# Kernel optimization log

Hardware: AMD Instinct MI355X
Metric: run time of the kernel (lower is better)

## Reference

```python
import jax, jax.numpy as jnp
from jax import lax
import numpy as np

HEAD_SIZE = 64
D_MIX = 32
D_DECAY = 64
D_GATE = 64


def setup_inputs() -> dict:
    key = jax.random.key(0)
    B, T, C = 4, 2048, 1024
    H = C // HEAD_SIZE
    ks = jax.random.split(key, 24)
    n = lambda i, shape, s=1.0: (jax.random.normal(ks[i], shape, dtype=jnp.float32) * s)
    return {
        "x": n(0, (B, T, C)),
        "maa_x": n(1, (C,), 0.1), "maa_w": n(2, (C,), 0.1), "maa_k": n(3, (C,), 0.1),
        "maa_v": n(4, (C,), 0.1), "maa_r": n(5, (C,), 0.1), "maa_g": n(6, (C,), 0.1),
        "maa_w1": n(7, (C, 5 * D_MIX), 0.01), "maa_w2": n(8, (5, D_MIX, C), 0.01),
        "Wr": n(9, (C, C), C ** -0.5), "Wk": n(10, (C, C), C ** -0.5),
        "Wv": n(11, (C, C), C ** -0.5), "Wo": n(12, (C, C), C ** -0.5),
        "gate_w1": n(13, (C, D_GATE), 0.01), "gate_w2": n(14, (D_GATE, C), 0.01),
        "time_decay": n(15, (C,), 1.0) - 4.0,
        "decay_w1": n(16, (C, D_DECAY), 0.01), "decay_w2": n(17, (D_DECAY, C), 0.01),
        "u": n(18, (H, HEAD_SIZE), 0.1),
        "ln_g": jnp.ones((C,), jnp.float32), "ln_b": jnp.zeros((C,), jnp.float32),
    }


def _wkv6(r, k, v, w, u):
    # r,k,v: [B,T,C]; w: decay (already exp(-exp(.))) [B,T,C]; u: [H,N]
    B, T, C = r.shape
    N = HEAD_SIZE
    H = C // N
    to_h = lambda a: a.reshape(B, T, H, N).transpose(1, 0, 2, 3)  # [T,B,H,N]
    rT, kT, vT, wT = map(to_h, (r, k, v, w))

    def step(S, inp):  # S: [B,H,N,N] (key_dim i x value_dim j)
        rt, kt, vt, wt = inp
        kv = kt[..., :, None] * vt[..., None, :]            # [B,H,N,N]
        y = jnp.einsum('bhi,bhij->bhj', rt, S + u[None, :, :, None] * kv)
        S = wt[..., None] * S + kv
        return S, y

    S0 = jnp.zeros((B, H, N, N), r.dtype)
    _, y = lax.scan(step, S0, (rT, kT, vT, wT))
    return y.transpose(1, 0, 2, 3).reshape(B, T, C)


def reference(x, maa_x, maa_w, maa_k, maa_v, maa_r, maa_g, maa_w1, maa_w2,
              Wr, Wk, Wv, Wo, gate_w1, gate_w2, time_decay, decay_w1, decay_w2,
              u, ln_g, ln_b):
    B, T, C = x.shape
    H, N = C // HEAD_SIZE, HEAD_SIZE
    # time shift: prepend zero row, drop last (ZeroPad2d((0,0,1,-1)))
    xx = jnp.concatenate([jnp.zeros_like(x[:, :1]), x[:, :-1]], axis=1) - x
    xxx = x + xx * maa_x
    lora = jnp.tanh(xxx @ maa_w1).reshape(B, T, 5, D_MIX)
    m = jnp.einsum('btfd,fdc->fbtc', lora, maa_w2)  # [5,B,T,C]
    mw, mk, mv, mr, mg = m[0], m[1], m[2], m[3], m[4]
    xw = x + xx * (maa_w + mw)
    xk = x + xx * (maa_k + mk)
    xv = x + xx * (maa_v + mv)
    xr = x + xx * (maa_r + mr)
    xg = x + xx * (maa_g + mg)
    r = xr @ Wr
    k = xk @ Wk
    v = xv @ Wv
    g = jnp.tanh(xg @ gate_w1) @ gate_w2
    w = time_decay + jnp.tanh(xw @ decay_w1) @ decay_w2
    wdec = jnp.exp(-jnp.exp(w))  # decay applied inside the CUDA kernel
    y = _wkv6(r, k, v, wdec, u)
    # GroupNorm over heads, eps = 1e-5 * HEAD_SIZE_DIVISOR**2 = 6.4e-4
    yh = y.reshape(B, T, H, N)
    mu = yh.mean(-1, keepdims=True)
    var = yh.var(-1, keepdims=True)
    yn = ((yh - mu) / jnp.sqrt(var + 6.4e-4)).reshape(B, T, C) * ln_g + ln_b
    return (yn * g) @ Wo
```

## Files before the change

### kernel.cpp

```cpp
#include <hip/hip_runtime.h>
#include <hip/hip_bf16.h>
#include <stdint.h>

typedef __hip_bfloat16 bf16;
typedef __attribute__((ext_vector_type(8))) short bf16x8;
typedef __attribute__((ext_vector_type(4))) float f32x4;

#define CC 1024
#define TT 2048
#define BB 4
#define BT 8192
#define HH 16
#define NN 64

#define MFMA(a, b, c) __builtin_amdgcn_mfma_f32_16x16x32_bf16(a, b, c, 0, 0, 0)

#define GLD(g, l) __builtin_amdgcn_global_load_lds( \
    (const __attribute__((address_space(1))) void*)(g), \
    (__attribute__((address_space(3))) void*)(l), 16, 0, 0)

__device__ __forceinline__ short f2bs(float f) {
    bf16 h = __float2bfloat16(f);
    return *reinterpret_cast<short*>(&h);
}
__device__ __forceinline__ float bs2f(short s) {
    bf16 h = *reinterpret_cast<bf16*>(&s);
    return __bfloat162float(h);
}

__device__ __forceinline__ size_t blk_idx(int m, int k, int ktiles) {
    return ((size_t)(m >> 8) * ktiles + (k >> 6)) * 16384
         + ((k >> 3) & 7) * 2048 + (m & 255) * 8 + (k & 7);
}

template <typename EPI>
__device__ __forceinline__ void gemm128(short* As, short* Bs,
                                        const bf16* __restrict__ A, int lda,
                                        const bf16* __restrict__ Bt, int ldb,
                                        int kiters, int m0, int n0, EPI epi)
{
    const int tid = threadIdx.x;
    const int l   = tid & 63, wv = tid >> 6;
    const int wm  = wv >> 1, wn = wv & 1;
    const int q   = l >> 4, lr = l & 15;
    const int row = tid & 127, kg1 = tid >> 7;

    f32x4 acc[4][4] = {};

    const bf16* ga = A  + (size_t)(m0 + row) * lda + kg1 * 8;
    const bf16* gb = Bt + (size_t)(n0 + row) * ldb + kg1 * 8;
    short* la1 = As + tid * 8;
    short* la2 = As + (tid + 256) * 8;
    short* lb1 = Bs + tid * 8;
    short* lb2 = Bs + (tid + 256) * 8;

    for (int kb = 0; kb < kiters; ++kb) {
        __syncthreads();
        const bf16* gak = ga + kb * 32;
        const bf16* gbk = gb + kb * 32;
        GLD(gak,      la1);
        GLD(gak + 16, la2);
        GLD(gbk,      lb1);
        GLD(gbk + 16, lb2);
        __syncthreads();
        bf16x8 af[4], bfb[4];
#pragma unroll
        for (int mt = 0; mt < 4; ++mt)
            af[mt] = *(const bf16x8*)(As + (q * 128 + wm * 64 + mt * 16 + lr) * 8);
#pragma unroll
        for (int nt = 0; nt < 4; ++nt)
            bfb[nt] = *(const bf16x8*)(Bs + (q * 128 + wn * 64 + nt * 16 + lr) * 8);
#pragma unroll
        for (int mt = 0; mt < 4; ++mt)
#pragma unroll
            for (int nt = 0; nt < 4; ++nt)
                acc[mt][nt] = MFMA(af[mt], bfb[nt], acc[mt][nt]);
    }
#pragma unroll
    for (int mt = 0; mt < 4; ++mt)
#pragma unroll
        for (int nt = 0; nt < 4; ++nt)
#pragma unroll
            for (int rr = 0; rr < 4; ++rr)
                epi(m0 + wm * 64 + mt * 16 + q * 4 + rr,
                    n0 + wn * 64 + nt * 16 + lr, acc[mt][nt][rr]);
}

template <typename EPI>
__device__ __forceinline__ void gemm128k64(short* As, short* Bs,
                                           const bf16* __restrict__ A, int lda,
                                           const bf16* __restrict__ Bt, int ldb,
                                           int kiters, int m0, int n0, EPI epi)
{
    const int tid = threadIdx.x;
    const int l   = tid & 63, wv = tid >> 6;
    const int wm  = wv >> 1, wn = wv & 1;
    const int q   = l >> 4, lr = l & 15;
    const int row = tid & 127, kg1 = tid >> 7;

    f32x4 acc[4][4] = {};

    const bf16* ga = A  + (size_t)(m0 + row) * lda + kg1 * 8;
    const bf16* gb = Bt + (size_t)(n0 + row) * ldb + kg1 * 8;

    auto stage = [&](int kb, int u) {
        const bf16* gak = ga + kb * 64;
        const bf16* gbk = gb + kb * 64;
        short* la = As + u * 8192 + tid * 8;
        short* lb = Bs + u * 8192 + tid * 8;
        GLD(gak,      la);
        GLD(gak + 16, la + 2048);
        GLD(gak + 32, la + 4096);
        GLD(gak + 48, la + 6144);
        GLD(gbk,      lb);
        GLD(gbk + 16, lb + 2048);
        GLD(gbk + 32, lb + 4096);
        GLD(gbk + 48, lb + 6144);
    };

    __syncthreads();
    stage(0, 0);
    __syncthreads();
    for (int kb = 0; kb < kiters; ++kb) {
        const int cur = kb & 1;
        if (kb + 1 < kiters) stage(kb + 1, cur ^ 1);
        const short* Ac = As + cur * 8192;
        const short* Bc = Bs + cur * 8192;
        bf16x8 af[2][4], bfb[2][4];
#pragma unroll
        for (int hh = 0; hh < 2; ++hh) {
#pragma unroll
            for (int mt = 0; mt < 4; ++mt)
                af[hh][mt] = *(const bf16x8*)(Ac +
                    ((q + hh * 4) * 128 + wm * 64 + mt * 16 + lr) * 8);
#pragma unroll
            for (int nt = 0; nt < 4; ++nt)
                bfb[hh][nt] = *(const bf16x8*)(Bc +
                    ((q + hh * 4) * 128 + wn * 64 + nt * 16 + lr) * 8);
        }
        __builtin_amdgcn_s_setprio(1);
#pragma unroll
        for (int mt = 0; mt < 4; ++mt)
#pragma unroll
            for (int nt = 0; nt < 4; ++nt) {
                acc[mt][nt] = MFMA(af[0][mt], bfb[0][nt], acc[mt][nt]);
                acc[mt][nt] = MFMA(af[1][mt], bfb[1][nt], acc[mt][nt]);
            }
        __builtin_amdgcn_s_setprio(0);
        __syncthreads();
    }
#pragma unroll
    for (int mt = 0; mt < 4; ++mt)
#pragma unroll
        for (int nt = 0; nt < 4; ++nt)
#pragma unroll
            for (int rr = 0; rr < 4; ++rr)
                epi(m0 + wm * 64 + mt * 16 + q * 4 + rr,
                    n0 + wn * 64 + nt * 16 + lr, acc[mt][nt][rr]);
}

template <typename EPI>
__device__ __forceinline__ void gemm256(short* As, short* Bs,
                                        const bf16* __restrict__ A,
                                        const bf16* __restrict__ Bt,
                                        int kiters, int m0, int n0, EPI epi)
{
    const int tid = threadIdx.x;
    const int l   = tid & 63, wv = tid >> 6;
    const int wm  = wv >> 2, wn = wv & 3;
    const int q   = l >> 4, lr = l & 15;

    f32x4 acc[8][4] = {};

    const bf16* ga = A  + (size_t)(m0 >> 8) * 16 * 16384 + tid * 8;
    const bf16* gb = Bt + (size_t)(n0 >> 8) * 16 * 16384 + tid * 8;

    auto stage = [&](int kb, int u) {
        const bf16* gak = ga + (size_t)kb * 16384;
        const bf16* gbk = gb + (size_t)kb * 16384;
        short* la = As + u * 16384 + tid * 8;
        short* lb = Bs + u * 16384 + tid * 8;
        GLD(gak,         la);
        GLD(gak + 4096,  la + 4096);
        GLD(gak + 8192,  la + 8192);
        GLD(gak + 12288, la + 12288);
        GLD(gbk,         lb);
        GLD(gbk + 4096,  lb + 4096);
        GLD(gbk + 8192,  lb + 8192);
        GLD(gbk + 12288, lb + 12288);
    };

    __syncthreads();
    stage(0, 0);
    __syncthreads();
    for (int kb = 0; kb < kiters; ++kb) {
        const int cur = kb & 1;
        if (kb + 1 < kiters) stage(kb + 1, cur ^ 1);
        const short* Ac = As + cur * 16384;
        const short* Bc = Bs + cur * 16384;
#pragma unroll
        for (int hh = 0; hh < 2; ++hh) {
            bf16x8 af[8], bfb[4];
#pragma unroll
            for (int mt = 0; mt < 8; ++mt)
                af[mt] = *(const bf16x8*)(Ac +
                    ((q + hh * 4) * 256 + wm * 128 + mt * 16 + lr) * 8);
#pragma unroll
            for (int nt = 0; nt < 4; ++nt)
                bfb[nt] = *(const bf16x8*)(Bc +
                    ((q + hh * 4) * 256 + wn * 64 + nt * 16 + lr) * 8);
            __builtin_amdgcn_s_setprio(1);
#pragma unroll
            for (int mt = 0; mt < 8; ++mt)
#pragma unroll
                for (int nt = 0; nt < 4; ++nt)
                    acc[mt][nt] = MFMA(af[mt], bfb[nt], acc[mt][nt]);
            __builtin_amdgcn_s_setprio(0);
        }
        __syncthreads();
    }
#pragma unroll
    for (int mt = 0; mt < 8; ++mt)
#pragma unroll
        for (int nt = 0; nt < 4; ++nt)
#pragma unroll
            for (int rr = 0; rr < 4; ++rr)
                epi(m0 + wm * 128 + mt * 16 + q * 4 + rr,
                    n0 + wn * 64 + nt * 16 + lr, acc[mt][nt][rr]);
}

template <typename EPI>
__device__ __forceinline__ void gemmHid(short* As, short* Bs,
                                        const bf16* __restrict__ A,
                                        const bf16* __restrict__ Bt, int ldb,
                                        int kiters, int m0, EPI epi)
{
    const int tid = threadIdx.x;
    const int l   = tid & 63, wv = tid >> 6;
    const int q   = l >> 4, lr = l & 15;
    const int row64 = tid & 63, kg8 = tid >> 6;

    f32x4 acc[2][4] = {};

    const bf16* ga = A + (size_t)(m0 >> 8) * 16 * 16384 + tid * 8;
    const bf16* gb = Bt + (size_t)row64 * ldb + kg8 * 8;

    auto stage = [&](int kb, int u) {
        const bf16* gak = ga + (size_t)kb * 16384;
        short* la = As + u * 16384 + tid * 8;
        GLD(gak,         la);
        GLD(gak + 4096,  la + 4096);
        GLD(gak + 8192,  la + 8192);
        GLD(gak + 12288, la + 12288);
        GLD(gb + kb * 64, Bs + u * 4096 + tid * 8);
    };

    __syncthreads();
    stage(0, 0);
    __syncthreads();
    for (int kb = 0; kb < kiters; ++kb) {
        const int cur = kb & 1;
        if (kb + 1 < kiters) stage(kb + 1, cur ^ 1);
        const short* Ac = As + cur * 16384;
        const short* Bc = Bs + cur * 4096;
        bf16x8 af[2][2], bfb[2][4];
#pragma unroll
        for (int hh = 0; hh < 2; ++hh) {
#pragma unroll
            for (int mt = 0; mt < 2; ++mt)
                af[hh][mt] = *(const bf16x8*)(Ac +
                    ((q + hh * 4) * 256 + wv * 32 + mt * 16 + lr) * 8);
#pragma unroll
            for (int nt = 0; nt < 4; ++nt)
                bfb[hh][nt] = *(const bf16x8*)(Bc +
                    ((q + hh * 4) * 64 + nt * 16 + lr) * 8);
        }
#pragma unroll
        for (int mt = 0; mt < 2; ++mt)
#pragma unroll
            for (int nt = 0; nt < 4; ++nt) {
                acc[mt][nt] = MFMA(af[0][mt], bfb[0][nt], acc[mt][nt]);
                acc[mt][nt] = MFMA(af[1][mt], bfb[1][nt], acc[mt][nt]);
            }
        __syncthreads();
    }
#pragma unroll
    for (int mt = 0; mt < 2; ++mt)
#pragma unroll
        for (int nt = 0; nt < 4; ++nt)
#pragma unroll
            for (int rr = 0; rr < 4; ++rr)
                epi(m0 + wv * 32 + mt * 16 + q * 4 + rr,
                    nt * 16 + lr, acc[mt][nt][rr]);
}

__global__ __launch_bounds__(256) void k_prep_all(
    const float* __restrict__ Wr, const float* __restrict__ Wk,
    const float* __restrict__ Wv, const float* __restrict__ Wo,
    const float* __restrict__ maa_w1, const float* __restrict__ gate_w1,
    const float* __restrict__ decay_w1, const float* __restrict__ gate_w2,
    const float* __restrict__ decay_w2, const float* __restrict__ maa_w2,
    const float* __restrict__ mw, const float* __restrict__ mk,
    const float* __restrict__ mv, const float* __restrict__ mr,
    const float* __restrict__ mg, const float* __restrict__ x,
    const float* __restrict__ maa_x,
    bf16* __restrict__ WT3, bf16* __restrict__ WoT, bf16* __restrict__ w1T,
    bf16* __restrict__ w1T2, bf16* __restrict__ w2T2, bf16* __restrict__ w2T5,
    float* __restrict__ maas, bf16* __restrict__ xxx,
    bf16* __restrict__ xb, bf16* __restrict__ xxb)
{
    __shared__ float tile[32][33];
    int idx = blockIdx.x;
    if (idx >= 4900) {
        size_t i = ((size_t)(idx - 4900) * 256 + threadIdx.x) * 4;
        int cc = i & (CC - 1);
        int t  = (i >> 10) & (TT - 1);
        float4 xm = *(const float4*)(x + i);
        float4 xp = t ? *(const float4*)(x + i - CC)
                      : make_float4(0.f, 0.f, 0.f, 0.f);
        float4 ax = *(const float4*)(maa_x + cc);
        float xxv[4] = {xp.x - xm.x, xp.y - xm.y, xp.z - xm.z, xp.w - xm.w};
        float xmv[4] = {xm.x, xm.y, xm.z, xm.w};
        float axv[4] = {ax.x, ax.y, ax.z, ax.w};
#pragma unroll
        for (int e = 0; e < 4; ++e) {
            xb[i + e]  = __float2bfloat16(xmv[e]);
            xxb[i + e] = __float2bfloat16(xxv[e]);
            xxx[i + e] = __float2bfloat16(xmv[e] + xxv[e] * axv[e]);
        }
        return;
    }
    const float* src; bf16* dst; int rows, cols_in, tx_;
    bool blocked = false;
    if (idx < 4096) {
        int s = idx >> 10; idx &= 1023;
        src = (s == 0) ? Wr : (s == 1) ? Wk : (s == 2) ? Wv : Wo;
        dst = (s == 3) ? WoT : WT3 + (size_t)s * CC * CC;
        blocked = (s != 3);
        rows = CC; cols_in = CC; tx_ = 32;
    } else if (idx < 4352) { idx -= 4096; src = maa_w1;  dst = w1T;  rows = CC; cols_in = 160; tx_ = 8; }
    else if (idx < 4480)   { idx -= 4352; src = gate_w1; dst = w1T2; rows = CC; cols_in = 64;  tx_ = 4; }
    else if (idx < 4608)   { idx -= 4480; src = decay_w1; dst = w1T2 + 128 * CC; rows = CC; cols_in = 64; tx_ = 4; }
    else if (idx < 4672)   { idx -= 4608; src = gate_w2;  dst = w2T2;           rows = 64; cols_in = CC; tx_ = 32; }
    else if (idx < 4736)   { idx -= 4672; src = decay_w2; dst = w2T2 + CC * 64; rows = 64; cols_in = CC; tx_ = 32; }
    else if (idx < 4896)   { idx -= 4736; int f = idx >> 5; idx &= 31;
                             src = maa_w2 + (size_t)f * 32 * CC;
                             dst = w2T5 + (size_t)f * CC * 32; rows = 32; cols_in = CC; tx_ = 32; }
    else {
        int i = (idx - 4896) * 256 + threadIdx.x;
        if (i < CC) {
            maas[i]          = mw[i];
            maas[CC + i]     = mk[i];
            maas[2 * CC + i] = mv[i];
            maas[3 * CC + i] = mr[i];
            maas[4 * CC + i] = mg[i];
        }
        return;
    }
    int bx = idx % tx_, by = idx / tx_;
    int c0 = bx * 32, r0 = by * 32;
    int tx = threadIdx.x & 31, ty = threadIdx.x >> 5;
    for (int i = ty; i < 32; i += 8) {
        int cc2 = c0 + tx;
        tile[i][tx] = (cc2 < cols_in) ? src[(size_t)(r0 + i) * cols_in + cc2] : 0.f;
    }
    __syncthreads();
    if (blocked) {
        for (int i = ty; i < 32; i += 8) {
            int R = c0 + i, C = r0 + tx;
            dst[blk_idx(R, C, 16)] = __float2bfloat16(tile[tx][i]);
        }
    } else {
        for (int i = ty; i < 32; i += 8)
            dst[(size_t)(c0 + i) * rows + r0 + tx] = __float2bfloat16(tile[tx][i]);
    }
}

__global__ __launch_bounds__(256) void g_lora(const bf16* __restrict__ xxx,
                                              const bf16* __restrict__ w1T,
                                              bf16* __restrict__ L)
{
    __shared__ __align__(16) short lds[8192];
    int m0 = blockIdx.x * 128, n0 = blockIdx.y * 128;
    gemm128(lds, lds + 4096, xxx, CC, w1T, CC, CC / 32, m0, n0,
            [&](int m, int n, float v) {
                if (n < 160) L[(size_t)m * 160 + n] = __float2bfloat16(tanhf(v));
            });
}

__global__ __launch_bounds__(256) void g_xvar(const bf16* __restrict__ L,
                                              const bf16* __restrict__ w2T,
                                              const float* __restrict__ maas,
                                              const bf16* __restrict__ xb,
                                              const bf16* __restrict__ xxb,
                                              bf16* __restrict__ xvars)
{
    __shared__ __align__(16) short lds[8192];
    int m0 = blockIdx.x * 128, n0 = blockIdx.y * 128;
    for (int f = 0; f < 5; ++f) {
        const bf16* A  = L + f * 32;
        const bf16* Bt = w2T + (size_t)f * CC * 32;
        const float* maa = maas + f * CC;
        bf16* out = xvars + (size_t)f * BT * CC;
        gemm128(lds, lds + 4096, A, 160, Bt, 32, 1, m0, n0,
                [&](int m, int n, float v) {
                    float xm = __bfloat162float(xb[(size_t)m * CC + n]);
                    float xx = __bfloat162float(xxb[(size_t)m * CC + n]);
                    out[blk_idx(m, n, 16)] =
                        __float2bfloat16(xm + xx * (maa[n] + v));
                });
    }
}

__global__ __launch_bounds__(512) void g_rkv5(const bf16* __restrict__ xvars,
                                              const bf16* __restrict__ WT,
                                              const bf16* __restrict__ w1T2,
                                              bf16* __restrict__ rkv,
                                              bf16* __restrict__ hid)
{
    __shared__ __align__(16) short lds[65536];
    int bid = blockIdx.x;
    if (bid < 384) {
        int swz = (bid & 7) * 48 + (bid >> 3);
        int z  = swz >> 7;
        int r2 = swz & 127;
        int n0 = (r2 >> 5) * 256;
        int m0 = (r2 & 31) * 256;
        int f = (z == 0) ? 3 : z;
        const bf16* A  = xvars + (size_t)f * BT * CC;
        const bf16* Bt = WT + (size_t)z * CC * CC;
        bf16* out = rkv + (size_t)z * BT * CC;
        gemm256(lds, lds + 32768, A, Bt, CC / 64, m0, n0,
                [&](int m, int n, float v) {
                    out[(size_t)m * CC + n] = __float2bfloat16(v);
                });
    } else {
        int hb = bid - 384;
        int zz = hb >> 5, mi = hb & 31;
        const bf16* A  = xvars + (size_t)(zz == 0 ? 4 : 0) * BT * CC;
        const bf16* Bt = w1T2 + (size_t)zz * 128 * CC;
        bf16* out = hid + (size_t)zz * BT * 64;
        gemmHid(lds, lds + 32768, A, Bt, CC, CC / 64, mi * 256,
                [&](int m, int n, float v) {
                    out[(size_t)m * 64 + n] = __float2bfloat16(tanhf(v));
                });
    }
}

__global__ __launch_bounds__(256) void k_wkv_p1(const bf16* __restrict__ r,
                                                const bf16* __restrict__ kk,
                                                const bf16* __restrict__ vv,
                                                const bf16* __restrict__ hidW,
                                                const bf16* __restrict__ w2d,
                                                const float* __restrict__ td,
                                                const float* __restrict__ u,
                                                bf16* __restrict__ y,
                                                bf16* __restrict__ RTg,
                                                short* __restrict__ Mg,
                                                float* __restrict__ plg)
{
    constexpr int PW = 65, PB = 72;
    __shared__ __align__(16) char smem[16640 + 3 * 9216 + 768];
    float* LW = (float*)smem;
    short* VT = (short*)smem;
    short* RT = (short*)(smem + 16640);
    short* KT = (short*)(smem + 16640 + 9216);
    short* AT = KT;
    short* KH = (short*)(smem + 16640 + 2 * 9216);
    short* HT = KT;
    short* WD = KH;
    float* SU = (float*)(smem + 16640 + 3 * 9216);
    float* SD = SU + 64;

    const int tid = threadIdx.x;
    const int lane = tid & 63, wq = tid >> 6;
    const int row = tid >> 2, g = tid & 3, j0 = g * 16;
    const int l15 = lane & 15, q = lane >> 4;
    const int bh = blockIdx.x >> 5, c = blockIdx.x & 31;
    const int b = bh >> 4, h = bh & 15;
    const size_t base = (size_t)b * TT * CC + (size_t)h * NN;
    const int t0 = c * 64;
    const int bt0 = b * TT + t0;
    const size_t cb = (size_t)blockIdx.x * 4096;

    if (tid < 64) SU[tid] = u[h * NN + tid];

#pragma unroll
    for (int rnd = 0; rnd < 2; ++rnd) {
        int ee = rnd * 256 + tid;
        int rw = ee >> 3, c8 = (ee & 7) * 8;
        *(bf16x8*)(HT + rw * PB + c8) =
            *(const bf16x8*)(hidW + (size_t)(bt0 + rw) * 64 + c8);
        *(bf16x8*)(WD + rw * PB + c8) =
            *(const bf16x8*)(w2d + (size_t)(h * 64 + rw) * 64 + c8);
    }
    const size_t gb = base + (size_t)(t0 + row) * CC + j0;
    bf16x8 r0 = *(const bf16x8*)(r + gb),  r1 = *(const bf16x8*)(r + gb + 8);
    bf16x8 k0 = *(const bf16x8*)(kk + gb), k1 = *(const bf16x8*)(kk + gb + 8);
    bf16x8 v0 = *(const bf16x8*)(vv + gb), v1 = *(const bf16x8*)(vv + gb + 8);
    float tdv[4];
#pragma unroll
    for (int ct = 0; ct < 4; ++ct) tdv[ct] = td[h * 64 + ct * 16 + l15];
    __syncthreads();
    {
        bf16x8 aH0 = *(const bf16x8*)(HT + (wq * 16 + l15) * PB + q * 8);
        bf16x8 aH1 = *(const bf16x8*)(HT + (wq * 16 + l15) * PB + q * 8 + 32);
        f32x4 lwa[4] = {};
#pragma unroll
        for (int ct = 0; ct < 4; ++ct) {
            bf16x8 bW0 = *(const bf16x8*)(WD + (ct * 16 + l15) * PB + q * 8);
            bf16x8 bW1 = *(const bf16x8*)(WD + (ct * 16 + l15) * PB + q * 8 + 32);
            lwa[ct] = MFMA(aH0, bW0, lwa[ct]);
            lwa[ct] = MFMA(aH1, bW1, lwa[ct]);
        }
#pragma unroll
        for (int ct = 0; ct < 4; ++ct)
#pragma unroll
            for (int rr = 0; rr < 4; ++rr) {
                int t = wq * 16 + q * 4 + rr, j = ct * 16 + l15;
                LW[t * PW + j] = -expf(tdv[ct] + lwa[ct][rr]);
            }
    }
    __syncthreads();
    for (int jj = 0; jj < 16; ++jj) {
        int j = wq * 16 + jj;
        float xv = LW[lane * PW + j];
#pragma unroll
        for (int d = 1; d < 64; d <<= 1) {
            float t2 = __shfl_up(xv, d);
            if (lane >= d) xv += t2;
        }
        LW[lane * PW + j] = xv;
    }
    __syncthreads();
    float rF[16], kF[16];
#pragma unroll
    for (int c2 = 0; c2 < 8; ++c2) {
        rF[c2] = bs2f(r0[c2]); rF[8 + c2] = bs2f(r1[c2]);
        kF[c2] = bs2f(k0[c2]); kF[8 + c2] = bs2f(k1[c2]);
    }
    float cwp[16], cwm[16], cwL[16];
#pragma unroll
    for (int c2 = 0; c2 < 16; ++c2) {
        cwp[c2] = LW[row * PW + j0 + c2];
        cwm[c2] = row ? LW[(row - 1) * PW + j0 + c2] : 0.f;
        cwL[c2] = LW[63 * PW + j0 + c2];
    }
    bf16x8 w0, w1;
#pragma unroll
    for (int c2 = 0; c2 < 8; ++c2) {
        w0[c2] = f2bs(rF[c2] * expf(cwm[c2]));
        w1[c2] = f2bs(rF[8 + c2] * expf(cwm[8 + c2]));
    }
    *(bf16x8*)(RT + row * PB + j0)     = w0;
    *(bf16x8*)(RT + row * PB + j0 + 8) = w1;
    *(bf16x8*)((short*)RTg + cb + row * 64 + j0)     = w0;
    *(bf16x8*)((short*)RTg + cb + row * 64 + j0 + 8) = w1;
#pragma unroll
    for (int c2 = 0; c2 < 8; ++c2) {
        w0[c2] = f2bs(kF[c2] * expf(-cwp[c2]));
        w1[c2] = f2bs(kF[8 + c2] * expf(-cwp[8 + c2]));
    }
    *(bf16x8*)(KT + row * PB + j0)     = w0;
    *(bf16x8*)(KT + row * PB + j0 + 8) = w1;
#pragma unroll
    for (int c2 = 0; c2 < 16; ++c2)
        KH[(j0 + c2) * PB + row] = f2bs(kF[c2] * expf(cwL[c2] - cwp[c2]));
    if (tid < 64) plg[(size_t)blockIdx.x * 64 + tid] = expf(LW[63 * PW + tid]);
    float dpart = 0.f;
#pragma unroll
    for (int c2 = 0; c2 < 16; ++c2)
        dpart = fmaf(rF[c2] * kF[c2], SU[j0 + c2], dpart);
    dpart += __shfl_xor(dpart, 1);
    dpart += __shfl_xor(dpart, 2);
    if (g == 0) SD[row] = dpart;
    __syncthreads();
#pragma unroll
    for (int c2 = 0; c2 < 8; ++c2) {
        VT[(j0 + c2) * PB + row]     = v0[c2];
        VT[(j0 + 8 + c2) * PB + row] = v1[c2];
    }
    bf16x8 aF0 = *(const bf16x8*)(RT + (wq * 16 + l15) * PB + q * 8);
    bf16x8 aF1 = *(const bf16x8*)(RT + (wq * 16 + l15) * PB + q * 8 + 32);
    f32x4 Am[4] = {};
#pragma unroll
    for (int ct = 0; ct < 4; ++ct) {
        bf16x8 bF0 = *(const bf16x8*)(KT + (ct * 16 + l15) * PB + q * 8);
        bf16x8 bF1 = *(const bf16x8*)(KT + (ct * 16 + l15) * PB + q * 8 + 32);
        Am[ct] = MFMA(aF0, bF0, Am[ct]);
        Am[ct] = MFMA(aF1, bF1, Am[ct]);
    }
    __syncthreads();
#pragma unroll
    for (int ct = 0; ct < 4; ++ct)
#pragma unroll
        for (int rr = 0; rr < 4; ++rr) {
            int s = wq * 16 + q * 4 + rr, p = ct * 16 + l15;
            float vA = Am[ct][rr];
            vA = (p > s) ? 0.f : (p == s ? SD[s] : vA);
            AT[s * PB + p] = f2bs(vA);
        }
    __syncthreads();
    f32x4 Y[4] = {}, M[4] = {};
    bf16x8 aA0 = *(const bf16x8*)(AT + (wq * 16 + l15) * PB + q * 8);
    bf16x8 aA1 = *(const bf16x8*)(AT + (wq * 16 + l15) * PB + q * 8 + 32);
    bf16x8 aV0 = *(const bf16x8*)(VT + (wq * 16 + l15) * PB + q * 8);
    bf16x8 aV1 = *(const bf16x8*)(VT + (wq * 16 + l15) * PB + q * 8 + 32);
#pragma unroll
    for (int ct = 0; ct < 4; ++ct) {
        bf16x8 bV0 = *(const bf16x8*)(VT + (ct * 16 + l15) * PB + q * 8);
        bf16x8 bV1 = *(const bf16x8*)(VT + (ct * 16 + l15) * PB + q * 8 + 32);
        Y[ct] = MFMA(aA0, bV0, Y[ct]);
        Y[ct] = MFMA(aA1, bV1, Y[ct]);
        bf16x8 bK0 = *(const bf16x8*)(KH + (ct * 16 + l15) * PB + q * 8);
        bf16x8 bK1 = *(const bf16x8*)(KH + (ct * 16 + l15) * PB + q * 8 + 32);
        M[ct] = MFMA(aV0, bK0, M[ct]);
        M[ct] = MFMA(aV1, bK1, M[ct]);
    }
#pragma unroll
    for (int ct = 0; ct < 4; ++ct)
#pragma unroll
        for (int rr = 0; rr < 4; ++rr) {
            int s = wq * 16 + q * 4 + rr;
            y[base + (size_t)(t0 + s) * CC + ct * 16 + l15] =
                __float2bfloat16(Y[ct][rr]);
            Mg[cb + (size_t)s * 64 + ct * 16 + l15] = f2bs(M[ct][rr]);
        }
}

__global__ __launch_bounds__(256) void k_wkv_p2(const short* __restrict__ Mg,
                                                const float* __restrict__ plg,
                                                bf16* __restrict__ Sg)
{
    int bh = blockIdx.x >> 4, part = blockIdx.x & 15;
    int i = part * 4 + (threadIdx.x >> 6), j = threadIdx.x & 63;
    float S = 0.f;
    size_t eb = (size_t)bh * 32 * 4096 + (size_t)i * 64 + j;
    size_t pb = (size_t)bh * 32 * 64 + j;
    for (int c = 0; c < 32; ++c) {
        Sg[eb + (size_t)c * 4096] = __float2bfloat16(S);
        S = plg[pb + (size_t)c * 64] * S + bs2f(Mg[eb + (size_t)c * 4096]);
    }
}

__global__ __launch_bounds__(256) void k_wkv_p3(const bf16* __restrict__ RTg,
                                                const bf16* __restrict__ Sg,
                                                const bf16* __restrict__ y,
                                                const bf16* __restrict__ hidG,
                                                const bf16* __restrict__ w2g,
                                                const float* __restrict__ ln_g,
                                                const float* __restrict__ ln_b,
                                                bf16* __restrict__ A2)
{
    constexpr int PB = 72;
    __shared__ __align__(16) short BufA[64 * PB], BufB[64 * PB];
    const int tid = threadIdx.x;
    const int lane = tid & 63, wq = tid >> 6;
    const int l15 = lane & 15, q = lane >> 4;
    const int bh = blockIdx.x >> 5, c = blockIdx.x & 31;
    const int b = bh >> 4, h = bh & 15;
    const int t0 = c * 64;
    const int bt0 = b * TT + t0;
    const size_t cb = (size_t)blockIdx.x * 4096;

#pragma unroll
    for (int rnd = 0; rnd < 2; ++rnd) {
        int ee = rnd * 256 + tid;
        int rw = ee >> 3, c8 = (ee & 7) * 8;
        *(bf16x8*)(BufA + rw * PB + c8) =
            *(const bf16x8*)(hidG + (size_t)(bt0 + rw) * 64 + c8);
        *(bf16x8*)(BufB + rw * PB + c8) =
            *(const bf16x8*)(w2g + (size_t)(h * 64 + rw) * 64 + c8);
    }
    __syncthreads();
    f32x4 G[4] = {};
    {
        bf16x8 aH0 = *(const bf16x8*)(BufA + (wq * 16 + l15) * PB + q * 8);
        bf16x8 aH1 = *(const bf16x8*)(BufA + (wq * 16 + l15) * PB + q * 8 + 32);
#pragma unroll
        for (int ct = 0; ct < 4; ++ct) {
            bf16x8 bW0 = *(const bf16x8*)(BufB + (ct * 16 + l15) * PB + q * 8);
            bf16x8 bW1 = *(const bf16x8*)(BufB + (ct * 16 + l15) * PB + q * 8 + 32);
            G[ct] = MFMA(aH0, bW0, G[ct]);
            G[ct] = MFMA(aH1, bW1, G[ct]);
        }
    }
    __syncthreads();
#pragma unroll
    for (int rnd = 0; rnd < 2; ++rnd) {
        int ee = rnd * 256 + tid;
        int rw = ee >> 3, c8 = (ee & 7) * 8;
        *(bf16x8*)(BufA + rw * PB + c8) =
            *(const bf16x8*)((const short*)RTg + cb + rw * 64 + c8);
        *(bf16x8*)(BufB + rw * PB + c8) =
            *(const bf16x8*)((const short*)Sg + cb + rw * 64 + c8);
    }
    __syncthreads();

    f32x4 Yc[4];
#pragma unroll
    for (int ct = 0; ct < 4; ++ct)
#pragma unroll
        for (int rr = 0; rr < 4; ++rr) {
            int s = wq * 16 + q * 4 + rr;
            Yc[ct][rr] = __bfloat162float(
                y[((size_t)bt0 + s) * CC + h * NN + ct * 16 + l15]);
        }
    bf16x8 aF0 = *(const bf16x8*)(BufA + (wq * 16 + l15) * PB + q * 8);
    bf16x8 aF1 = *(const bf16x8*)(BufA + (wq * 16 + l15) * PB + q * 8 + 32);
#pragma unroll
    for (int ct = 0; ct < 4; ++ct) {
        bf16x8 bS0 = *(const bf16x8*)(BufB + (ct * 16 + l15) * PB + q * 8);
        bf16x8 bS1 = *(const bf16x8*)(BufB + (ct * 16 + l15) * PB + q * 8 + 32);
        Yc[ct] = MFMA(aF0, bS0, Yc[ct]);
        Yc[ct] = MFMA(aF1, bS1, Yc[ct]);
    }
#pragma unroll
    for (int rr = 0; rr < 4; ++rr) {
        float s1 = 0.f, s2 = 0.f;
#pragma unroll
        for (int ct = 0; ct < 4; ++ct) {
            float vA = Yc[ct][rr];
            s1 += vA; s2 += vA * vA;
        }
#pragma unroll
        for (int o = 1; o < 16; o <<= 1) {
            s1 += __shfl_xor(s1, o);
            s2 += __shfl_xor(s2, o);
        }
        float mu  = s1 * (1.f / 64.f);
        float var = s2 * (1.f / 64.f) - mu * mu;
        float rstd = rsqrtf(var + 6.4e-4f);
        int s = wq * 16 + q * 4 + rr;
        size_t mrow = ((size_t)bt0 + s) * CC;
#pragma unroll
        for (int ct = 0; ct < 4; ++ct) {
            int ch = h * NN + ct * 16 + l15;
            float yn = (Yc[ct][rr] - mu) * rstd;
            float out = (yn * ln_g[ch] + ln_b[ch]) * G[ct][rr];
            A2[mrow + ch] = __float2bfloat16(out);
        }
    }
}

__global__ __launch_bounds__(256) void g_out(const bf16* __restrict__ A2,
                                             const bf16* __restrict__ WoT,
                                             float* __restrict__ out)
{
    __shared__ __align__(16) short lds[32768];
    int m0 = blockIdx.x * 128, n0 = blockIdx.y * 128;
    gemm128k64(lds, lds + 16384, A2, CC, WoT, CC, CC / 64, m0, n0,
               [&](int m, int n, float v) { out[(size_t)m * CC + n] = v; });
}

extern "C" void kernel_launch(void* const* d_in, const int* in_sizes, int n_in,
                              void* d_out, int out_size, void* d_ws, size_t ws_size,
                              hipStream_t stream)
{
    const float* x        = (const float*)d_in[0];
    const float* maa_x    = (const float*)d_in[1];
    const float* maa_w    = (const float*)d_in[2];
    const float* maa_k    = (const float*)d_in[3];
    const float* maa_v    = (const float*)d_in[4];
    const float* maa_r    = (const float*)d_in[5];
    const float* maa_g    = (const float*)d_in[6];
    const float* maa_w1   = (const float*)d_in[7];
    const float* maa_w2   = (const float*)d_in[8];
    const float* Wr       = (const float*)d_in[9];
    const float* Wk       = (const float*)d_in[10];
    const float* Wv       = (const float*)d_in[11];
    const float* Wo       = (const float*)d_in[12];
    const float* gate_w1  = (const float*)d_in[13];
    const float* gate_w2  = (const float*)d_in[14];
    const float* time_dec = (const float*)d_in[15];
    const float* decay_w1 = (const float*)d_in[16];
    const float* decay_w2 = (const float*)d_in[17];
    const float* u        = (const float*)d_in[18];
    const float* ln_g     = (const float*)d_in[19];
    const float* ln_b     = (const float*)d_in[20];

    size_t off = 0;
    auto alloc = [&](size_t bytes) {
        off = (off + 255) & ~(size_t)255;
        void* p = (char*)d_ws + off;
        off += bytes;
        return p;
    };
    bf16*  WT3   = (bf16*) alloc(3ull * CC * CC * 2);
    bf16*  WoT   = (bf16*) alloc((size_t)CC * CC * 2);
    bf16*  w1T   = (bf16*) alloc(256ull * CC * 2);
    bf16*  w1T2  = (bf16*) alloc(2ull * 128 * CC * 2);
    bf16*  w2T2  = (bf16*) alloc(2ull * CC * 64 * 2);
    bf16*  w2T5  = (bf16*) alloc(5ull * CC * 32 * 2);
    float* maas  = (float*)alloc(5ull * CC * 4);
    char* bufA = (char*)alloc((size_t)BT * CC * 2);
    bf16* xxxbf = (bf16*)bufA;
    bf16* A2    = (bf16*)bufA;
    char* bufB = (char*)alloc((size_t)BT * 160 * 2);
    bf16* Lbf  = (bf16*)bufB;
    bf16* hid  = (bf16*)bufB;
    char* bufC = (char*)alloc(5ull * BT * CC * 2);
    bf16*  xvars = (bf16*)bufC;
    bf16*  ybuf  = (bf16*)bufC;
    bf16*  RTg   = (bf16*)(bufC + (size_t)BT * CC * 2);
    bf16*  rkv  = (bf16*)alloc(3ull * BT * CC * 2);
    bf16*  Sg   = rkv;
    bf16*  xb   = (bf16*) alloc((size_t)BT * CC * 2);
    bf16*  xxb  = (bf16*) alloc((size_t)BT * CC * 2);
    short* Mg   = (short*)alloc(64ull * 32 * 4096 * 2);
    float* plg  = (float*)alloc(64ull * 32 * 64 * 4);

    k_prep_all<<<dim3(13092), 256, 0, stream>>>(
        Wr, Wk, Wv, Wo, maa_w1, gate_w1, decay_w1, gate_w2, decay_w2, maa_w2,
        maa_w, maa_k, maa_v, maa_r, maa_g, x, maa_x,
        WT3, WoT, w1T, w1T2, w2T2, w2T5, maas, xxxbf, xb, xxb);

    g_lora<<<dim3(64, 2), 256, 0, stream>>>(xxxbf, w1T, Lbf);
    g_xvar<<<dim3(64, 8), 256, 0, stream>>>(Lbf, w2T5, maas, xb, xxb, xvars);
    g_rkv5<<<dim3(448), 512, 0, stream>>>(xvars, WT3, w1T2, rkv, hid);
    k_wkv_p1<<<dim3(2048), 256, 0, stream>>>(rkv, rkv + (size_t)BT * CC,
                                             rkv + 2ull * BT * CC,
                                             hid + (size_t)BT * 64,
                                             w2T2 + CC * 64,
                                             time_dec, u, ybuf, RTg, Mg, plg);
    k_wkv_p2<<<dim3(1024), 256, 0, stream>>>(Mg, plg, Sg);
    k_wkv_p3<<<dim3(2048), 256, 0, stream>>>(RTg, Sg, ybuf,
                                             hid,
                                             w2T2,
                                             ln_g, ln_b, A2);
    g_out<<<dim3(64, 8), 256, 0, stream>>>(A2, WoT, (float*)d_out);
}
```

Baseline: 380.8 us.

## Prefetch two stages ahead in GEMMs with explicit vmcnt waits and raw barriers

Restructures the double-buffered LDS pipeline in all three GEMM helpers. Both buffers are now issued up front, and the next-next stage is issued after the post-compute barrier. Each iteration uses a partial s_waitcnt vmcnt so only the current stage's loads are awaited, instead of full __syncthreads drains. This lets global-to-LDS loads overlap the MFMA work more fully. The risks are correctness hazards: hand-counted vmcnt values must match the loads per stage, and the leading __syncthreads that guarded LDS reuse between calls has been removed.

```diff
diff --git a/kernel.cpp b/kernel.cpp
--- a/kernel.cpp
+++ b/kernel.cpp
@@ -118,12 +118,13 @@
         GLD(gbk + 48, lb + 6144);
     };
 
-    __syncthreads();
     stage(0, 0);
-    __syncthreads();
+    if (kiters > 1) stage(1, 1);
     for (int kb = 0; kb < kiters; ++kb) {
         const int cur = kb & 1;
-        if (kb + 1 < kiters) stage(kb + 1, cur ^ 1);
+        if (kb + 1 < kiters) asm volatile("s_waitcnt vmcnt(8)" ::: "memory");
+        else                 asm volatile("s_waitcnt vmcnt(0)" ::: "memory");
+        __builtin_amdgcn_s_barrier();
         const short* Ac = As + cur * 8192;
         const short* Bc = Bs + cur * 8192;
         bf16x8 af[2][4], bfb[2][4];
@@ -147,7 +148,8 @@
                 acc[mt][nt] = MFMA(af[1][mt], bfb[1][nt], acc[mt][nt]);
             }
         __builtin_amdgcn_s_setprio(0);
-        __syncthreads();
+        __builtin_amdgcn_s_barrier();
+        if (kb + 2 < kiters) stage(kb + 2, cur);
     }
 #pragma unroll
     for (int mt = 0; mt < 4; ++mt)
@@ -190,12 +192,13 @@
         GLD(gbk + 12288, lb + 12288);
     };
 
-    __syncthreads();
     stage(0, 0);
-    __syncthreads();
+    if (kiters > 1) stage(1, 1);
     for (int kb = 0; kb < kiters; ++kb) {
         const int cur = kb & 1;
-        if (kb + 1 < kiters) stage(kb + 1, cur ^ 1);
+        if (kb + 1 < kiters) asm volatile("s_waitcnt vmcnt(8)" ::: "memory");
+        else                 asm volatile("s_waitcnt vmcnt(0)" ::: "memory");
+        __builtin_amdgcn_s_barrier();
         const short* Ac = As + cur * 16384;
         const short* Bc = Bs + cur * 16384;
 #pragma unroll
@@ -217,7 +220,8 @@
                     acc[mt][nt] = MFMA(af[mt], bfb[nt], acc[mt][nt]);
             __builtin_amdgcn_s_setprio(0);
         }
-        __syncthreads();
+        __builtin_amdgcn_s_barrier();
+        if (kb + 2 < kiters) stage(kb + 2, cur);
     }
 #pragma unroll
     for (int mt = 0; mt < 8; ++mt)
@@ -255,12 +259,13 @@
         GLD(gb + kb * 64, Bs + u * 4096 + tid * 8);
     };
 
-    __syncthreads();
     stage(0, 0);
-    __syncthreads();
+    if (kiters > 1) stage(1, 1);
     for (int kb = 0; kb < kiters; ++kb) {
         const int cur = kb & 1;
-        if (kb + 1 < kiters) stage(kb + 1, cur ^ 1);
+        if (kb + 1 < kiters) asm volatile("s_waitcnt vmcnt(5)" ::: "memory");
+        else                 asm volatile("s_waitcnt vmcnt(0)" ::: "memory");
+        __builtin_amdgcn_s_barrier();
         const short* Ac = As + cur * 16384;
         const short* Bc = Bs + cur * 4096;
         bf16x8 af[2][2], bfb[2][4];
@@ -282,7 +287,8 @@
                 acc[mt][nt] = MFMA(af[0][mt], bfb[0][nt], acc[mt][nt]);
                 acc[mt][nt] = MFMA(af[1][mt], bfb[1][nt], acc[mt][nt]);
             }
-        __syncthreads();
+        __builtin_amdgcn_s_barrier();
+        if (kb + 2 < kiters) stage(kb + 2, cur);
     }
 #pragma unroll
     for (int mt = 0; mt < 2; ++mt)
```

Result: no change. 386.4 us (+1.5%).

## Store r/k/v head-blocked and pre-block GEMM operands for contiguous tile loads

Applied to the files above, without the earlier changes.

The r/k/v projection epilogue now writes its output head-major ([B*H, T, 64]), so the WKV kernels read contiguous 64-element rows instead of strided slices of the full channel dimension. The y buffer follows the same layout. The normed, gated activations A2 and the transposed Wo are written in a 128x64 tile-blocked order, which lets the output GEMM stage each K tile with fully contiguous global-to-LDS loads. The cost is scattered writes in the producer epilogues and a fixed layout coupling between kernels.

```diff
diff --git a/kernel.cpp b/kernel.cpp
--- a/kernel.cpp
+++ b/kernel.cpp
@@ -31,6 +31,16 @@
 __device__ __forceinline__ size_t blk_idx(int m, int k, int ktiles) {
     return ((size_t)(m >> 8) * ktiles + (k >> 6)) * 16384
          + ((k >> 3) & 7) * 2048 + (m & 255) * 8 + (k & 7);
+}
+
+__device__ __forceinline__ size_t blk128_idx(int m, int k, int ktiles) {
+    return ((size_t)(m >> 7) * ktiles + (k >> 6)) * 8192
+         + ((k >> 3) & 7) * 1024 + (m & 127) * 8 + (k & 7);
+}
+
+__device__ __forceinline__ size_t hb_idx(int m, int n) {
+    return ((((size_t)(m >> 11) << 4) + (n >> 6)) * 2048 + (m & 2047)) * 64
+         + (n & 63);
 }
 
 template <typename EPI>
@@ -87,35 +97,34 @@
 }
 
 template <typename EPI>
-__device__ __forceinline__ void gemm128k64(short* As, short* Bs,
-                                           const bf16* __restrict__ A, int lda,
-                                           const bf16* __restrict__ Bt, int ldb,
-                                           int kiters, int m0, int n0, EPI epi)
+__device__ __forceinline__ void gemm128b(short* As, short* Bs,
+                                         const bf16* __restrict__ A,
+                                         const bf16* __restrict__ Bt,
+                                         int kiters, int m0, int n0, EPI epi)
 {
     const int tid = threadIdx.x;
     const int l   = tid & 63, wv = tid >> 6;
     const int wm  = wv >> 1, wn = wv & 1;
     const int q   = l >> 4, lr = l & 15;
-    const int row = tid & 127, kg1 = tid >> 7;
 
     f32x4 acc[4][4] = {};
 
-    const bf16* ga = A  + (size_t)(m0 + row) * lda + kg1 * 8;
-    const bf16* gb = Bt + (size_t)(n0 + row) * ldb + kg1 * 8;
+    const bf16* ga = A  + (size_t)(m0 >> 7) * 16 * 8192 + tid * 8;
+    const bf16* gb = Bt + (size_t)(n0 >> 7) * 16 * 8192 + tid * 8;
 
     auto stage = [&](int kb, int u) {
-        const bf16* gak = ga + kb * 64;
-        const bf16* gbk = gb + kb * 64;
+        const bf16* gak = ga + (size_t)kb * 8192;
+        const bf16* gbk = gb + (size_t)kb * 8192;
         short* la = As + u * 8192 + tid * 8;
         short* lb = Bs + u * 8192 + tid * 8;
-        GLD(gak,      la);
-        GLD(gak + 16, la + 2048);
-        GLD(gak + 32, la + 4096);
-        GLD(gak + 48, la + 6144);
-        GLD(gbk,      lb);
-        GLD(gbk + 16, lb + 2048);
-        GLD(gbk + 32, lb + 4096);
-        GLD(gbk + 48, lb + 6144);
+        GLD(gak,        la);
+        GLD(gak + 2048, la + 2048);
+        GLD(gak + 4096, la + 4096);
+        GLD(gak + 6144, la + 6144);
+        GLD(gbk,        lb);
+        GLD(gbk + 2048, lb + 2048);
+        GLD(gbk + 4096, lb + 4096);
+        GLD(gbk + 6144, lb + 6144);
     };
 
     __syncthreads();
@@ -331,12 +340,12 @@
         return;
     }
     const float* src; bf16* dst; int rows, cols_in, tx_;
-    bool blocked = false;
+    int blkmode = 0;
     if (idx < 4096) {
         int s = idx >> 10; idx &= 1023;
         src = (s == 0) ? Wr : (s == 1) ? Wk : (s == 2) ? Wv : Wo;
         dst = (s == 3) ? WoT : WT3 + (size_t)s * CC * CC;
-        blocked = (s != 3);
+        blkmode = (s == 3) ? 2 : 1;
         rows = CC; cols_in = CC; tx_ = 32;
     } else if (idx < 4352) { idx -= 4096; src = maa_w1;  dst = w1T;  rows = CC; cols_in = 160; tx_ = 8; }
     else if (idx < 4480)   { idx -= 4352; src = gate_w1; dst = w1T2; rows = CC; cols_in = 64;  tx_ = 4; }
@@ -365,10 +374,15 @@
         tile[i][tx] = (cc2 < cols_in) ? src[(size_t)(r0 + i) * cols_in + cc2] : 0.f;
     }
     __syncthreads();
-    if (blocked) {
+    if (blkmode == 1) {
         for (int i = ty; i < 32; i += 8) {
             int R = c0 + i, C = r0 + tx;
             dst[blk_idx(R, C, 16)] = __float2bfloat16(tile[tx][i]);
+        }
+    } else if (blkmode == 2) {
+        for (int i = ty; i < 32; i += 8) {
+            int R = c0 + i, C = r0 + tx;
+            dst[blk128_idx(R, C, 16)] = __float2bfloat16(tile[tx][i]);
         }
     } else {
         for (int i = ty; i < 32; i += 8)
@@ -432,7 +446,7 @@
         bf16* out = rkv + (size_t)z * BT * CC;
         gemm256(lds, lds + 32768, A, Bt, CC / 64, m0, n0,
                 [&](int m, int n, float v) {
-                    out[(size_t)m * CC + n] = __float2bfloat16(v);
+                    out[hb_idx(m, n)] = __float2bfloat16(v);
                 });
     } else {
         int hb = bid - 384;
@@ -478,9 +492,9 @@
     const int l15 = lane & 15, q = lane >> 4;
     const int bh = blockIdx.x >> 5, c = blockIdx.x & 31;
     const int b = bh >> 4, h = bh & 15;
-    const size_t base = (size_t)b * TT * CC + (size_t)h * NN;
     const int t0 = c * 64;
     const int bt0 = b * TT + t0;
+    const size_t hbb = (size_t)bh * TT * NN;
     const size_t cb = (size_t)blockIdx.x * 4096;
 
     if (tid < 64) SU[tid] = u[h * NN + tid];
@@ -494,7 +508,7 @@
         *(bf16x8*)(WD + rw * PB + c8) =
             *(const bf16x8*)(w2d + (size_t)(h * 64 + rw) * 64 + c8);
     }
-    const size_t gb = base + (size_t)(t0 + row) * CC + j0;
+    const size_t gb = hbb + (size_t)(t0 + row) * 64 + j0;
     bf16x8 r0 = *(const bf16x8*)(r + gb),  r1 = *(const bf16x8*)(r + gb + 8);
     bf16x8 k0 = *(const bf16x8*)(kk + gb), k1 = *(const bf16x8*)(kk + gb + 8);
     bf16x8 v0 = *(const bf16x8*)(vv + gb), v1 = *(const bf16x8*)(vv + gb + 8);
@@ -622,7 +636,7 @@
 #pragma unroll
         for (int rr = 0; rr < 4; ++rr) {
             int s = wq * 16 + q * 4 + rr;
-            y[base + (size_t)(t0 + s) * CC + ct * 16 + l15] =
+            y[hbb + (size_t)(t0 + s) * 64 + ct * 16 + l15] =
                 __float2bfloat16(Y[ct][rr]);
             Mg[cb + (size_t)s * 64 + ct * 16 + l15] = f2bs(M[ct][rr]);
         }
@@ -661,6 +675,7 @@
     const int b = bh >> 4, h = bh & 15;
     const int t0 = c * 64;
     const int bt0 = b * TT + t0;
+    const size_t hbb = (size_t)bh * TT * NN;
     const size_t cb = (size_t)blockIdx.x * 4096;
 
 #pragma unroll
@@ -704,7 +719,7 @@
         for (int rr = 0; rr < 4; ++rr) {
             int s = wq * 16 + q * 4 + rr;
             Yc[ct][rr] = __bfloat162float(
-                y[((size_t)bt0 + s) * CC + h * NN + ct * 16 + l15]);
+                y[hbb + (size_t)(t0 + s) * 64 + ct * 16 + l15]);
         }
     bf16x8 aF0 = *(const bf16x8*)(BufA + (wq * 16 + l15) * PB + q * 8);
     bf16x8 aF1 = *(const bf16x8*)(BufA + (wq * 16 + l15) * PB + q * 8 + 32);
@@ -732,13 +747,12 @@
         float var = s2 * (1.f / 64.f) - mu * mu;
         float rstd = rsqrtf(var + 6.4e-4f);
         int s = wq * 16 + q * 4 + rr;
-        size_t mrow = ((size_t)bt0 + s) * CC;
 #pragma unroll
         for (int ct = 0; ct < 4; ++ct) {
             int ch = h * NN + ct * 16 + l15;
             float yn = (Yc[ct][rr] - mu) * rstd;
             float out = (yn * ln_g[ch] + ln_b[ch]) * G[ct][rr];
-            A2[mrow + ch] = __float2bfloat16(out);
+            A2[blk128_idx(bt0 + s, ch, 16)] = __float2bfloat16(out);
         }
     }
 }
@@ -749,8 +763,8 @@
 {
     __shared__ __align__(16) short lds[32768];
     int m0 = blockIdx.x * 128, n0 = blockIdx.y * 128;
-    gemm128k64(lds, lds + 16384, A2, CC, WoT, CC, CC / 64, m0, n0,
-               [&](int m, int n, float v) { out[(size_t)m * CC + n] = v; });
+    gemm128b(lds, lds + 16384, A2, WoT, CC / 64, m0, n0,
+             [&](int m, int n, float v) { out[(size_t)m * CC + n] = v; });
 }
 
 extern "C" void kernel_launch(void* const* d_in, const int* in_sizes, int n_in,
```

Result: slower. 394.2 us (+3.5%).
